# Kernel optimization log

Hardware: AMD Instinct MI355X
Metric: run time of the kernel (lower is better)

## Reference

```python
import jax, jax.numpy as jnp
import numpy as np

B, N, G, E = 4, 8192, 512, 512
D = 3 * E  # fused channel dim = 1536
BN_EPS = 1e-5


def setup_inputs() -> dict:
    key = jax.random.key(0)
    ks = jax.random.split(key, 8)
    f32 = jnp.float32
    return {
        "xyz": jax.random.normal(ks[0], (B, N, 3), f32),
        "centers": jax.random.normal(ks[1], (B, G, 3), f32),
        "H4": jax.random.normal(ks[2], (B, G, E), f32),
        "H8": jax.random.normal(ks[3], (B, G, E), f32),
        "H12": jax.random.normal(ks[4], (B, G, E), f32),
        "w1": jax.random.normal(ks[5], (512, D), f32) * 0.02,
        "b1": jnp.zeros((512,), f32),
        "g1": jnp.ones((512,), f32),
        "be1": jnp.zeros((512,), f32),
        "m1": jnp.zeros((512,), f32),
        "v1": jnp.ones((512,), f32),
        "w2": jax.random.normal(ks[6], (512, 512), f32) * 0.02,
        "b2": jnp.zeros((512,), f32),
        "g2": jnp.ones((512,), f32),
        "be2": jnp.zeros((512,), f32),
        "m2": jnp.zeros((512,), f32),
        "v2": jnp.ones((512,), f32),
    }


def _bn(x, gamma, beta, mean, var):
    # BatchNorm1d, eval mode with running stats (per-channel, last axis)
    return (x - mean) * jax.lax.rsqrt(var + BN_EPS) * gamma + beta


def reference(xyz, centers, H4, H8, H12,
              w1, b1, g1, be1, m1, v1,
              w2, b2, g2, be2, m2, v2):
    fused = jnp.concatenate([H4, H8, H12], axis=-1)  # [B,G,D]
    # squared pairwise distances [B,N,G]
    d = (jnp.sum(xyz * xyz, axis=-1, keepdims=True)
         + jnp.sum(centers * centers, axis=-1)[:, None, :]
         - 2.0 * jnp.einsum('bnc,bgc->bng', xyz, centers))
    neg_d3, idx = jax.lax.top_k(-d, 3)  # 3 smallest distances, ascending
    d3 = -neg_d3  # [B,N,3]
    recip = 1.0 / (d3 + 1e-8)
    w = recip / jnp.sum(recip, axis=-1, keepdims=True)  # [B,N,3]
    # gather neighbor features: [B,N,3,D]
    gathered = jax.vmap(lambda f, i: f[i])(fused, idx)
    interp = jnp.einsum('bnk,bnkd->bnd', w, gathered)  # [B,N,D]
    # 1x1 conv == per-point linear; conv -> BN(eval) -> ReLU, twice
    h = jax.nn.relu(_bn(interp @ w1.T + b1, g1, be1, m1, v1))
    h = jax.nn.relu(_bn(h @ w2.T + b2, g2, be2, m2, v2))
    return h  # [B,N,512]
```

## Files before the change

kernel.cpp:

```cpp
#include <hip/hip_runtime.h>
#include <stdint.h>

#define NP 8192
#define NG 512
#define DF 1536

using f32x4    = __attribute__((ext_vector_type(4))) float;
using bf16x8   = __attribute__((ext_vector_type(8))) __bf16;
using ushort8v = __attribute__((ext_vector_type(8))) unsigned short;


__device__ __forceinline__ unsigned short f32_to_bf16(float f) {
  unsigned int u = __float_as_uint(f);
  u += 0x7fffu + ((u >> 16) & 1u);
  return (unsigned short)(u >> 16);
}
__device__ __forceinline__ float bf2f(unsigned short u) {
  return __uint_as_float(((unsigned)u) << 16);
}

struct FusedArgs {
  const float *xyz, *centers, *H4, *H8, *H12, *w1, *w2;
  const float *g1, *be1, *m1, *v1, *g2, *be2, *m2, *v2, *b1, *b2;
  unsigned short *fswz, *w1s, *w2s, *Amatb;
  int *nidx; float *nw, *s1, *t1, *s2, *t2;
  float *outp;
};

__device__ void phase_knn(const FusedArgs& a, char* smem, int w) {
  const int tid = threadIdx.x;
  float4* cs = (float4*)smem;
  const int b = w >> 7;
  for (int i = tid; i < NG; i += 256) {
    float c0 = a.centers[((size_t)b * NG + i) * 3 + 0];
    float c1 = a.centers[((size_t)b * NG + i) * 3 + 1];
    float c2 = a.centers[((size_t)b * NG + i) * 3 + 2];
    float4 v; v.x = c0; v.y = c1; v.z = c2; v.w = c0 * c0 + c1 * c1 + c2 * c2;
    cs[(i >> 7) * 129 + (i & 127)] = v;
  }
  __syncthreads();
  const int t = (w & 127) * 256 + tid;
  const int p = t >> 2, q = t & 3;
  const size_t pi = (size_t)b * NP + p;
  const float x0 = a.xyz[pi * 3 + 0], x1 = a.xyz[pi * 3 + 1], x2 = a.xyz[pi * 3 + 2];
  const float xx = x0 * x0 + x1 * x1 + x2 * x2;
  float d0 = 3.4e38f, d1 = 3.4e38f, d2 = 3.4e38f;
  int i0 = 0, i1 = 0, i2 = 0;
  const int gbase = q * 128;
  const float4* csq = cs + q * 129;
#pragma unroll 4
  for (int j = 0; j < 128; ++j) {
    float4 c = csq[j];
    float d = xx + c.w - 2.0f * (x0 * c.x + x1 * c.y + x2 * c.z);
    int g = gbase + j;
    bool c0 = d < d0, c1 = d < d1, c2 = d < d2;
    float nd2 = c1 ? d1 : (c2 ? d : d2); int ni2 = c1 ? i1 : (c2 ? g : i2);
    float nd1 = c0 ? d0 : (c1 ? d : d1); int ni1 = c0 ? i0 : (c1 ? g : i1);
    d0 = c0 ? d : d0;                    i0 = c0 ? g : i0;
    d1 = nd1; i1 = ni1; d2 = nd2; i2 = ni2;
  }
#pragma unroll
  for (int off = 1; off <= 2; off <<= 1) {
    float e0 = __shfl_xor(d0, off), e1 = __shfl_xor(d1, off), e2 = __shfl_xor(d2, off);
    int j0 = __shfl_xor(i0, off), j1 = __shfl_xor(i1, off), j2 = __shfl_xor(i2, off);
#pragma unroll
    for (int s = 0; s < 3; ++s) {
      float e = (s == 0) ? e0 : (s == 1 ? e1 : e2);
      int   j = (s == 0) ? j0 : (s == 1 ? j1 : j2);
      bool c0 = (e < d0) || (e == d0 && j < i0);
      bool c1 = (e < d1) || (e == d1 && j < i1);
      bool c2 = (e < d2) || (e == d2 && j < i2);
      float nd2 = c1 ? d1 : (c2 ? e : d2); int ni2 = c1 ? i1 : (c2 ? j : i2);
      float nd1 = c0 ? d0 : (c1 ? e : d1); int ni1 = c0 ? i0 : (c1 ? j : i1);
      d0 = c0 ? e : d0;                    i0 = c0 ? j : i0;
      d1 = nd1; i1 = ni1; d2 = nd2; i2 = ni2;
    }
  }
  if (q == 0) {
    float r0 = 1.0f / (d0 + 1e-8f), r1 = 1.0f / (d1 + 1e-8f), r2 = 1.0f / (d2 + 1e-8f);
    float inv = 1.0f / (r0 + r1 + r2);
    a.nw[pi * 3 + 0] = r0 * inv; a.nw[pi * 3 + 1] = r1 * inv; a.nw[pi * 3 + 2] = r2 * inv;
    a.nidx[pi * 3 + 0] = i0; a.nidx[pi * 3 + 1] = i1; a.nidx[pi * 3 + 2] = i2;
  }
}

__device__ void phase_casts(const FusedArgs& a, int u) {
  const int tid = threadIdx.x;
  if (u < 2048) {
    const int qd = (u - 512) * 256 + tid;
    const int L = qd & 63, t2 = qd >> 6;
    const int kc = t2 % 48, mg = t2 / 48;
    const int m = mg * 16 + (L & 15);
    const int k = kc * 32 + (L >> 4) * 8;
    const float* src = (k < 512) ? a.H4 : (k < 1024 ? a.H8 : a.H12);
    const float* sp = &src[(size_t)m * 512 + (k & 511)];
    float4 va = *(const float4*)sp, vb = *(const float4*)(sp + 4);
    ushort8v o;
    o[0] = f32_to_bf16(va.x); o[1] = f32_to_bf16(va.y);
    o[2] = f32_to_bf16(va.z); o[3] = f32_to_bf16(va.w);
    o[4] = f32_to_bf16(vb.x); o[5] = f32_to_bf16(vb.y);
    o[6] = f32_to_bf16(vb.z); o[7] = f32_to_bf16(vb.w);
    *(ushort8v*)&a.fswz[((size_t)(mg * 48 + kc)) * 512 + L * 8] = o;
  } else if (u < 2432) {
    const int qd = (u - 2048) * 256 + tid;
    const int L = qd & 63, t2 = qd >> 6;
    const int kc = t2 % 48, ng = t2 / 48;
    const int n = ng * 16 + (L & 15);
    const int k = kc * 32 + (L >> 4) * 8;
    const float* sp = &a.w1[(size_t)n * 1536 + k];
    float4 va = *(const float4*)sp, vb = *(const float4*)(sp + 4);
    ushort8v o;
    o[0] = f32_to_bf16(va.x); o[1] = f32_to_bf16(va.y);
    o[2] = f32_to_bf16(va.z); o[3] = f32_to_bf16(va.w);
    o[4] = f32_to_bf16(vb.x); o[5] = f32_to_bf16(vb.y);
    o[6] = f32_to_bf16(vb.z); o[7] = f32_to_bf16(vb.w);
    *(ushort8v*)&a.w1s[((size_t)(ng * 48 + kc)) * 512 + L * 8] = o;
  } else if (u < 2560) {
    const int qd = (u - 2432) * 256 + tid;
    const int L = qd & 63, t2 = qd >> 6;
    const int kc = t2 & 15, ng = t2 >> 4;
    const int n = ng * 16 + (L & 15);
    const int k = kc * 32 + (L >> 4) * 8;
    const float* sp = &a.w2[(size_t)n * 512 + k];
    float4 va = *(const float4*)sp, vb = *(const float4*)(sp + 4);
    ushort8v o;
    o[0] = f32_to_bf16(va.x); o[1] = f32_to_bf16(va.y);
    o[2] = f32_to_bf16(va.z); o[3] = f32_to_bf16(va.w);
    o[4] = f32_to_bf16(vb.x); o[5] = f32_to_bf16(vb.y);
    o[6] = f32_to_bf16(vb.z); o[7] = f32_to_bf16(vb.w);
    *(ushort8v*)&a.w2s[((size_t)(ng * 16 + kc)) * 512 + L * 8] = o;
  } else {
    for (int i = tid; i < 512; i += 256) {
      float sa = a.g1[i] / sqrtf(a.v1[i] + 1e-5f);
      a.s1[i] = sa; a.t1[i] = a.be1[i] - a.m1[i] * sa;
      float sb = a.g2[i] / sqrtf(a.v2[i] + 1e-5f);
      a.s2[i] = sb; a.t2[i] = a.be2[i] - a.m2[i] * sb;
    }
  }
}

__device__ void phase_gemm1(const FusedArgs& a, char* smem, int blk) {
  float* red = (float*)smem;
  const int tid = threadIdx.x, lane = tid & 63, wv = tid >> 6;
  const int m0 = (blk >> 3) * 32;
  const int n0 = (blk & 7) * 64;
  const unsigned short* Ap = a.fswz + ((size_t)(m0 >> 4) * 48 + wv * 12) * 512 + lane * 8;
  const unsigned short* Bp = a.w1s  + ((size_t)(n0 >> 4) * 48 + wv * 12) * 512 + lane * 8;

  f32x4 acc[2][4];
#pragma unroll
  for (int i = 0; i < 2; ++i)
#pragma unroll
    for (int j = 0; j < 4; ++j) acc[i][j] = (f32x4){0.f, 0.f, 0.f, 0.f};

  bf16x8 af[2], bfr[4], afn[2], bfn[4];
#pragma unroll
  for (int i = 0; i < 2; ++i)
    af[i]  = __builtin_bit_cast(bf16x8, *(const ushort8v*)(Ap + (size_t)i * 48 * 512));
#pragma unroll
  for (int i = 0; i < 4; ++i)
    bfr[i] = __builtin_bit_cast(bf16x8, *(const ushort8v*)(Bp + (size_t)i * 48 * 512));
#pragma unroll 1
  for (int kc = 0; kc < 12; ++kc) {
    if (kc < 11) {
#pragma unroll
      for (int i = 0; i < 2; ++i)
        afn[i] = __builtin_bit_cast(bf16x8, *(const ushort8v*)(Ap + (size_t)i * 48 * 512 + (kc + 1) * 512));
#pragma unroll
      for (int i = 0; i < 4; ++i)
        bfn[i] = __builtin_bit_cast(bf16x8, *(const ushort8v*)(Bp + (size_t)i * 48 * 512 + (kc + 1) * 512));
    }
#pragma unroll
    for (int mi = 0; mi < 2; ++mi)
#pragma unroll
      for (int ni = 0; ni < 4; ++ni)
        acc[mi][ni] = __builtin_amdgcn_mfma_f32_16x16x32_bf16(af[mi], bfr[ni], acc[mi][ni], 0, 0, 0);
#pragma unroll
    for (int i = 0; i < 2; ++i) af[i] = afn[i];
#pragma unroll
    for (int i = 0; i < 4; ++i) bfr[i] = bfn[i];
  }

  for (int w = 0; w < 4; ++w) {
    if (wv == w) {
#pragma unroll
      for (int mi = 0; mi < 2; ++mi)
#pragma unroll
        for (int ni = 0; ni < 4; ++ni) {
          int col = ni * 16 + (lane & 15);
#pragma unroll
          for (int r = 0; r < 4; ++r) {
            int row = mi * 16 + (lane >> 4) * 4 + r;
            if (w == 0) red[row * 65 + col] = acc[mi][ni][r];
            else        red[row * 65 + col] += acc[mi][ni][r];
          }
        }
    }
    __syncthreads();
  }
  const int row = tid >> 3;
  const int col = (tid & 7) * 8;
  ushort8v o;
#pragma unroll
  for (int j = 0; j < 8; ++j) {
    int n = n0 + col + j;
    float v = red[row * 65 + col + j];
    o[j] = f32_to_bf16(a.s1[n] * (v + a.b1[n]) + a.t1[n]);
  }
  *(ushort8v*)&a.Amatb[(size_t)(m0 + row) * 512 + n0 + col] = o;
}

__global__ __launch_bounds__(512, 4) void k_mega(FusedArgs a) {
  __shared__ __align__(16) unsigned short hl[64 * 512];
  const int tid = threadIdx.x, lane = tid & 63, wv = tid >> 6;
  const int xcd = blockIdx.x & 7, slot = blockIdx.x >> 3;
  const int m0 = (xcd * 64 + slot) * 64;

  {
    const int rg = wv & 3, kc0 = (wv >> 2) * 8;
    const int p = m0 + rg * 16 + (lane & 15);
    const int b = p >> 13;
    const int i0 = a.nidx[p * 3 + 0], i1 = a.nidx[p * 3 + 1], i2 = a.nidx[p * 3 + 2];
    const float w0 = a.nw[p * 3 + 0], w1v = a.nw[p * 3 + 1], w2v = a.nw[p * 3 + 2];
    const int co = kc0 * 32 + (lane >> 4) * 8;
    const unsigned short* A0 = a.Amatb + ((size_t)(b * 512 + i0)) * 512 + co;
    const unsigned short* A1 = a.Amatb + ((size_t)(b * 512 + i1)) * 512 + co;
    const unsigned short* A2 = a.Amatb + ((size_t)(b * 512 + i2)) * 512 + co;
    unsigned short* wp = hl + (size_t)(rg * 16 + kc0) * 512 + lane * 8;
#pragma unroll 4
    for (int j = 0; j < 8; ++j) {
      ushort8v u0 = *(const ushort8v*)(A0 + j * 32);
      ushort8v u1 = *(const ushort8v*)(A1 + j * 32);
      ushort8v u2 = *(const ushort8v*)(A2 + j * 32);
      ushort8v o;
#pragma unroll
      for (int jj = 0; jj < 8; ++jj) {
        float v = w0 * bf2f(u0[jj]) + w1v * bf2f(u1[jj]) + w2v * bf2f(u2[jj]);
        o[jj] = f32_to_bf16(fmaxf(v, 0.f));
      }
      *(ushort8v*)(wp + (size_t)j * 512) = o;
    }
  }
  __syncthreads();

  const int n0 = wv * 64;
  const unsigned short* Bbase = a.w2s + (size_t)(n0 >> 4) * 16 * 512 + lane * 8;

  f32x4 acc[4][4];
#pragma unroll
  for (int i = 0; i < 4; ++i)
#pragma unroll
    for (int j = 0; j < 4; ++j) acc[i][j] = (f32x4){0.f, 0.f, 0.f, 0.f};

  bf16x8 bfr[4], bfn[4];
#pragma unroll
  for (int ni = 0; ni < 4; ++ni)
    bfr[ni] = __builtin_bit_cast(bf16x8,
        *(const ushort8v*)(Bbase + (size_t)(ni * 16) * 512));
#pragma unroll 1
  for (int kc = 0; kc < 16; ++kc) {
    if (kc < 15) {
#pragma unroll
      for (int ni = 0; ni < 4; ++ni)
        bfn[ni] = __builtin_bit_cast(bf16x8,
            *(const ushort8v*)(Bbase + (size_t)(ni * 16 + kc + 1) * 512));
    }
    bf16x8 af[4];
#pragma unroll
    for (int mi = 0; mi < 4; ++mi)
      af[mi] = __builtin_bit_cast(bf16x8,
          *(const ushort8v*)(hl + (size_t)(mi * 16 + kc) * 512 + lane * 8));
#pragma unroll
    for (int mi = 0; mi < 4; ++mi)
#pragma unroll
      for (int ni = 0; ni < 4; ++ni)
        acc[mi][ni] = __builtin_amdgcn_mfma_f32_16x16x32_bf16(
            af[mi], bfr[ni], acc[mi][ni], 0, 0, 0);
#pragma unroll
    for (int ni = 0; ni < 4; ++ni) bfr[ni] = bfn[ni];
  }

#pragma unroll
  for (int mi = 0; mi < 4; ++mi) {
    int mbase = m0 + mi * 16 + (lane >> 4) * 4;
#pragma unroll
    for (int ni = 0; ni < 4; ++ni) {
      int n = n0 + ni * 16 + (lane & 15);
      float s = a.s2[n], bb = a.b2[n], t = a.t2[n];
      f32x4 v = acc[mi][ni];
#pragma unroll
      for (int r = 0; r < 4; ++r)
        __builtin_nontemporal_store(fmaxf(s * (v[r] + bb) + t, 0.f),
                                    &a.outp[(size_t)(mbase + r) * 512 + n]);
    }
  }
}

__global__ __launch_bounds__(256) void k_casts(FusedArgs a) {
  phase_casts(a, 512 + blockIdx.x);
}
__global__ __launch_bounds__(256) void k_g1knn(FusedArgs a) {
  __shared__ __align__(16) char smem[8448];
  if (blockIdx.x < 512) phase_gemm1(a, smem, blockIdx.x);
  else                  phase_knn(a, smem, blockIdx.x - 512);
}

extern "C" void kernel_launch(void* const* d_in, const int* in_sizes, int n_in,
                              void* d_out, int out_size, void* d_ws, size_t ws_size,
                              hipStream_t stream) {
  char* ws = (char*)d_ws;
  FusedArgs a;
  a.xyz     = (const float*)d_in[0];
  a.centers = (const float*)d_in[1];
  a.H4      = (const float*)d_in[2];
  a.H8      = (const float*)d_in[3];
  a.H12     = (const float*)d_in[4];
  a.w1      = (const float*)d_in[5];
  a.b1      = (const float*)d_in[6];
  a.g1      = (const float*)d_in[7];
  a.be1     = (const float*)d_in[8];
  a.m1      = (const float*)d_in[9];
  a.v1      = (const float*)d_in[10];
  a.w2      = (const float*)d_in[11];
  a.b2      = (const float*)d_in[12];
  a.g2      = (const float*)d_in[13];
  a.be2     = (const float*)d_in[14];
  a.m2      = (const float*)d_in[15];
  a.v2      = (const float*)d_in[16];
  a.fswz  = (unsigned short*)(ws);
  a.w1s   = (unsigned short*)(ws + 6291456);
  a.w2s   = (unsigned short*)(ws + 7864320);
  a.Amatb = (unsigned short*)(ws + 8388608);
  a.nidx  = (int*)           (ws + 10485760);
  a.nw    = (float*)         (ws + 10878976);
  a.s1    = (float*)         (ws + 11272192);
  a.t1 = a.s1 + 512; a.s2 = a.t1 + 512; a.t2 = a.s2 + 512;
  a.outp  = (float*)d_out;

  k_casts<<<2049, 256, 0, stream>>>(a);
  k_g1knn<<<1024, 256, 0, stream>>>(a);
  k_mega <<< 512, 512, 0, stream>>>(a);
}
```

Before: 162.4 us.

## Fuse bf16 casts into GEMM1 loads and merge cast kernel into pre kernel

Drops the separate cast kernel that converted H4/H8/H12 and w1 to swizzled bf16 buffers. GEMM1 now loads fp32 directly from the inputs and packs to bf16 in registers, and it computes BN1 scale and shift inline. The w2 cast is folded into the same launch as GEMM1 and KNN, cutting one kernel launch and the round trip through workspace memory. The cross-wave reduction now writes into separate per-wave LDS slices followed by a single barrier, instead of a serialized accumulate with four barriers. In exchange it uses more shared memory and issues uncoalesced strided fp32 loads with no prefetch, doubling the bytes loaded per element.

Result: slower. 174.4 us (+7.4%).

```diff
diff --git a/kernel.cpp b/kernel.cpp
--- a/kernel.cpp
+++ b/kernel.cpp
@@ -18,12 +18,20 @@
 __device__ __forceinline__ float bf2f(unsigned short u) {
   return __uint_as_float(((unsigned)u) << 16);
 }
+__device__ __forceinline__ bf16x8 pack8(float4 a, float4 b) {
+  ushort8v o;
+  o[0] = f32_to_bf16(a.x); o[1] = f32_to_bf16(a.y);
+  o[2] = f32_to_bf16(a.z); o[3] = f32_to_bf16(a.w);
+  o[4] = f32_to_bf16(b.x); o[5] = f32_to_bf16(b.y);
+  o[6] = f32_to_bf16(b.z); o[7] = f32_to_bf16(b.w);
+  return __builtin_bit_cast(bf16x8, o);
+}
 
 struct FusedArgs {
   const float *xyz, *centers, *H4, *H8, *H12, *w1, *w2;
   const float *g1, *be1, *m1, *v1, *g2, *be2, *m2, *v2, *b1, *b2;
-  unsigned short *fswz, *w1s, *w2s, *Amatb;
-  int *nidx; float *nw, *s1, *t1, *s2, *t2;
+  unsigned short *w2s, *Amatb;
+  int *nidx; float *nw, *s2, *t2;
   float *outp;
 };
 
@@ -84,68 +92,13 @@
   }
 }
 
-__device__ void phase_casts(const FusedArgs& a, int u) {
-  const int tid = threadIdx.x;
-  if (u < 2048) {
-    const int qd = (u - 512) * 256 + tid;
-    const int L = qd & 63, t2 = qd >> 6;
-    const int kc = t2 % 48, mg = t2 / 48;
-    const int m = mg * 16 + (L & 15);
-    const int k = kc * 32 + (L >> 4) * 8;
-    const float* src = (k < 512) ? a.H4 : (k < 1024 ? a.H8 : a.H12);
-    const float* sp = &src[(size_t)m * 512 + (k & 511)];
-    float4 va = *(const float4*)sp, vb = *(const float4*)(sp + 4);
-    ushort8v o;
-    o[0] = f32_to_bf16(va.x); o[1] = f32_to_bf16(va.y);
-    o[2] = f32_to_bf16(va.z); o[3] = f32_to_bf16(va.w);
-    o[4] = f32_to_bf16(vb.x); o[5] = f32_to_bf16(vb.y);
-    o[6] = f32_to_bf16(vb.z); o[7] = f32_to_bf16(vb.w);
-    *(ushort8v*)&a.fswz[((size_t)(mg * 48 + kc)) * 512 + L * 8] = o;
-  } else if (u < 2432) {
-    const int qd = (u - 2048) * 256 + tid;
-    const int L = qd & 63, t2 = qd >> 6;
-    const int kc = t2 % 48, ng = t2 / 48;
-    const int n = ng * 16 + (L & 15);
-    const int k = kc * 32 + (L >> 4) * 8;
-    const float* sp = &a.w1[(size_t)n * 1536 + k];
-    float4 va = *(const float4*)sp, vb = *(const float4*)(sp + 4);
-    ushort8v o;
-    o[0] = f32_to_bf16(va.x); o[1] = f32_to_bf16(va.y);
-    o[2] = f32_to_bf16(va.z); o[3] = f32_to_bf16(va.w);
-    o[4] = f32_to_bf16(vb.x); o[5] = f32_to_bf16(vb.y);
-    o[6] = f32_to_bf16(vb.z); o[7] = f32_to_bf16(vb.w);
-    *(ushort8v*)&a.w1s[((size_t)(ng * 48 + kc)) * 512 + L * 8] = o;
-  } else if (u < 2560) {
-    const int qd = (u - 2432) * 256 + tid;
-    const int L = qd & 63, t2 = qd >> 6;
-    const int kc = t2 & 15, ng = t2 >> 4;
-    const int n = ng * 16 + (L & 15);
-    const int k = kc * 32 + (L >> 4) * 8;
-    const float* sp = &a.w2[(size_t)n * 512 + k];
-    float4 va = *(const float4*)sp, vb = *(const float4*)(sp + 4);
-    ushort8v o;
-    o[0] = f32_to_bf16(va.x); o[1] = f32_to_bf16(va.y);
-    o[2] = f32_to_bf16(va.z); o[3] = f32_to_bf16(va.w);
-    o[4] = f32_to_bf16(vb.x); o[5] = f32_to_bf16(vb.y);
-    o[6] = f32_to_bf16(vb.z); o[7] = f32_to_bf16(vb.w);
-    *(ushort8v*)&a.w2s[((size_t)(ng * 16 + kc)) * 512 + L * 8] = o;
-  } else {
-    for (int i = tid; i < 512; i += 256) {
-      float sa = a.g1[i] / sqrtf(a.v1[i] + 1e-5f);
-      a.s1[i] = sa; a.t1[i] = a.be1[i] - a.m1[i] * sa;
-      float sb = a.g2[i] / sqrtf(a.v2[i] + 1e-5f);
-      a.s2[i] = sb; a.t2[i] = a.be2[i] - a.m2[i] * sb;
-    }
-  }
-}
-
 __device__ void phase_gemm1(const FusedArgs& a, char* smem, int blk) {
   float* red = (float*)smem;
   const int tid = threadIdx.x, lane = tid & 63, wv = tid >> 6;
   const int m0 = (blk >> 3) * 32;
   const int n0 = (blk & 7) * 64;
-  const unsigned short* Ap = a.fswz + ((size_t)(m0 >> 4) * 48 + wv * 12) * 512 + lane * 8;
-  const unsigned short* Bp = a.w1s  + ((size_t)(n0 >> 4) * 48 + wv * 12) * 512 + lane * 8;
+  const int r16 = lane & 15;
+  const int k8  = (lane >> 4) * 8;
 
   f32x4 acc[2][4];
 #pragma unroll
@@ -153,61 +106,96 @@
 #pragma unroll
     for (int j = 0; j < 4; ++j) acc[i][j] = (f32x4){0.f, 0.f, 0.f, 0.f};
 
-  bf16x8 af[2], bfr[4], afn[2], bfn[4];
-#pragma unroll
-  for (int i = 0; i < 2; ++i)
-    af[i]  = __builtin_bit_cast(bf16x8, *(const ushort8v*)(Ap + (size_t)i * 48 * 512));
-#pragma unroll
-  for (int i = 0; i < 4; ++i)
-    bfr[i] = __builtin_bit_cast(bf16x8, *(const ushort8v*)(Bp + (size_t)i * 48 * 512));
+  const size_t arow0 = (size_t)(m0 + r16) * 512;
+  const size_t arow1 = (size_t)(m0 + 16 + r16) * 512;
+  const float* brow0 = a.w1 + (size_t)(n0 +  0 + r16) * 1536;
+  const float* brow1 = a.w1 + (size_t)(n0 + 16 + r16) * 1536;
+  const float* brow2 = a.w1 + (size_t)(n0 + 32 + r16) * 1536;
+  const float* brow3 = a.w1 + (size_t)(n0 + 48 + r16) * 1536;
+
 #pragma unroll 1
-  for (int kc = 0; kc < 12; ++kc) {
-    if (kc < 11) {
-#pragma unroll
-      for (int i = 0; i < 2; ++i)
-        afn[i] = __builtin_bit_cast(bf16x8, *(const ushort8v*)(Ap + (size_t)i * 48 * 512 + (kc + 1) * 512));
-#pragma unroll
-      for (int i = 0; i < 4; ++i)
-        bfn[i] = __builtin_bit_cast(bf16x8, *(const ushort8v*)(Bp + (size_t)i * 48 * 512 + (kc + 1) * 512));
-    }
+  for (int t = 0; t < 12; ++t) {
+    const int kc = wv * 12 + t;
+    const int ks = kc * 32 + k8;
+    const float* srcA = (ks < 512) ? a.H4 : (ks < 1024 ? a.H8 : a.H12);
+    const int kcol = ks & 511;
+    float4 a00 = *(const float4*)(srcA + arow0 + kcol);
+    float4 a01 = *(const float4*)(srcA + arow0 + kcol + 4);
+    float4 a10 = *(const float4*)(srcA + arow1 + kcol);
+    float4 a11 = *(const float4*)(srcA + arow1 + kcol + 4);
+    float4 b00 = *(const float4*)(brow0 + ks);
+    float4 b01 = *(const float4*)(brow0 + ks + 4);
+    float4 b10 = *(const float4*)(brow1 + ks);
+    float4 b11 = *(const float4*)(brow1 + ks + 4);
+    float4 b20 = *(const float4*)(brow2 + ks);
+    float4 b21 = *(const float4*)(brow2 + ks + 4);
+    float4 b30 = *(const float4*)(brow3 + ks);
+    float4 b31 = *(const float4*)(brow3 + ks + 4);
+    bf16x8 afr[2], bfr[4];
+    afr[0] = pack8(a00, a01); afr[1] = pack8(a10, a11);
+    bfr[0] = pack8(b00, b01); bfr[1] = pack8(b10, b11);
+    bfr[2] = pack8(b20, b21); bfr[3] = pack8(b30, b31);
 #pragma unroll
     for (int mi = 0; mi < 2; ++mi)
 #pragma unroll
       for (int ni = 0; ni < 4; ++ni)
-        acc[mi][ni] = __builtin_amdgcn_mfma_f32_16x16x32_bf16(af[mi], bfr[ni], acc[mi][ni], 0, 0, 0);
-#pragma unroll
-    for (int i = 0; i < 2; ++i) af[i] = afn[i];
-#pragma unroll
-    for (int i = 0; i < 4; ++i) bfr[i] = bfn[i];
-  }
-
-  for (int w = 0; w < 4; ++w) {
-    if (wv == w) {
-#pragma unroll
-      for (int mi = 0; mi < 2; ++mi)
-#pragma unroll
-        for (int ni = 0; ni < 4; ++ni) {
-          int col = ni * 16 + (lane & 15);
-#pragma unroll
-          for (int r = 0; r < 4; ++r) {
-            int row = mi * 16 + (lane >> 4) * 4 + r;
-            if (w == 0) red[row * 65 + col] = acc[mi][ni][r];
-            else        red[row * 65 + col] += acc[mi][ni][r];
-          }
-        }
-    }
-    __syncthreads();
-  }
+        acc[mi][ni] = __builtin_amdgcn_mfma_f32_16x16x32_bf16(afr[mi], bfr[ni], acc[mi][ni], 0, 0, 0);
+  }
+
+  float* redw = red + wv * 2080;
+#pragma unroll
+  for (int mi = 0; mi < 2; ++mi)
+#pragma unroll
+    for (int ni = 0; ni < 4; ++ni) {
+      const int col = ni * 16 + r16;
+      const int rowb = mi * 16 + (lane >> 4) * 4;
+#pragma unroll
+      for (int r = 0; r < 4; ++r)
+        redw[(rowb + r) * 65 + col] = acc[mi][ni][r];
+    }
+  __syncthreads();
   const int row = tid >> 3;
   const int col = (tid & 7) * 8;
   ushort8v o;
 #pragma unroll
   for (int j = 0; j < 8; ++j) {
-    int n = n0 + col + j;
-    float v = red[row * 65 + col + j];
-    o[j] = f32_to_bf16(a.s1[n] * (v + a.b1[n]) + a.t1[n]);
+    const int n = n0 + col + j;
+    float v = red[row * 65 + col + j] + red[2080 + row * 65 + col + j]
+            + red[4160 + row * 65 + col + j] + red[6240 + row * 65 + col + j];
+    float sa = a.g1[n] / sqrtf(a.v1[n] + 1e-5f);
+    float ta = a.be1[n] - a.m1[n] * sa;
+    o[j] = f32_to_bf16(sa * (v + a.b1[n]) + ta);
   }
   *(ushort8v*)&a.Amatb[(size_t)(m0 + row) * 512 + n0 + col] = o;
+}
+
+__device__ void phase_w2cast(const FusedArgs& a, int u2) {
+  const int tid = threadIdx.x;
+  if (u2 < 128) {
+    const int qd = u2 * 256 + tid;
+    const int L = qd & 63, t2 = qd >> 6;
+    const int kcb = t2 & 15, ng = t2 >> 4;
+    const int n = ng * 16 + (L & 15);
+    const int k = kcb * 32 + (L >> 4) * 8;
+    const float* sp = &a.w2[(size_t)n * 512 + k];
+    float4 va = *(const float4*)sp, vb = *(const float4*)(sp + 4);
+    bf16x8 o = pack8(va, vb);
+    *(ushort8v*)&a.w2s[((size_t)(ng * 16 + kcb)) * 512 + L * 8] =
+        __builtin_bit_cast(ushort8v, o);
+  } else {
+    for (int i = tid; i < 512; i += 256) {
+      float sb = a.g2[i] / sqrtf(a.v2[i] + 1e-5f);
+      a.s2[i] = sb; a.t2[i] = a.be2[i] - a.m2[i] * sb;
+    }
+  }
+}
+
+__global__ __launch_bounds__(256) void k_pre(FusedArgs a) {
+  __shared__ __align__(16) char smem[33280];
+  const int blk = blockIdx.x;
+  if (blk < 512)       phase_gemm1(a, smem, blk);
+  else if (blk < 1024) phase_knn(a, smem, blk - 512);
+  else                 phase_w2cast(a, blk - 1024);
 }
 
 __global__ __launch_bounds__(512, 4) void k_mega(FusedArgs a) {
@@ -294,15 +282,6 @@
                                     &a.outp[(size_t)(mbase + r) * 512 + n]);
     }
   }
-}
-
-__global__ __launch_bounds__(256) void k_casts(FusedArgs a) {
-  phase_casts(a, 512 + blockIdx.x);
-}
-__global__ __launch_bounds__(256) void k_g1knn(FusedArgs a) {
-  __shared__ __align__(16) char smem[8448];
-  if (blockIdx.x < 512) phase_gemm1(a, smem, blockIdx.x);
-  else                  phase_knn(a, smem, blockIdx.x - 512);
 }
 
 extern "C" void kernel_launch(void* const* d_in, const int* in_sizes, int n_in,
@@ -327,17 +306,14 @@
   a.be2     = (const float*)d_in[14];
   a.m2      = (const float*)d_in[15];
   a.v2      = (const float*)d_in[16];
-  a.fswz  = (unsigned short*)(ws);
-  a.w1s   = (unsigned short*)(ws + 6291456);
-  a.w2s   = (unsigned short*)(ws + 7864320);
-  a.Amatb = (unsigned short*)(ws + 8388608);
-  a.nidx  = (int*)           (ws + 10485760);
-  a.nw    = (float*)         (ws + 10878976);
-  a.s1    = (float*)         (ws + 11272192);
-  a.t1 = a.s1 + 512; a.s2 = a.t1 + 512; a.t2 = a.s2 + 512;
+  a.w2s   = (unsigned short*)(ws);
+  a.Amatb = (unsigned short*)(ws +  524288);
+  a.nidx  = (int*)           (ws + 2621440);
+  a.nw    = (float*)         (ws + 3014656);
+  a.s2    = (float*)         (ws + 3407872);
+  a.t2    = a.s2 + 512;
   a.outp  = (float*)d_out;
 
-  k_casts<<<2049, 256, 0, stream>>>(a);
-  k_g1knn<<<1024, 256, 0, stream>>>(a);
-  k_mega <<< 512, 512, 0, stream>>>(a);
-}
+  k_pre <<<1153, 256, 0, stream>>>(a);
+  k_mega<<< 512, 512, 0, stream>>>(a);
+}
```
